# Kernel optimization log

Measured on AMD Instinct MI355X. Metric: run time of the kernel, lower is better.

Reference implementation:

```python
import jax, jax.numpy as jnp
import numpy as np


def kernel_mus(n_kernels):
    l_mu = [1.0]
    if n_kernels == 1:
        return l_mu
    bin_size = 2.0 / (n_kernels - 1)
    l_mu.append(1 - bin_size / 2)
    for i in range(1, n_kernels - 1):
        l_mu.append(l_mu[i] - bin_size)
    return l_mu


def kernel_sigmas(n_kernels):
    bin_size = 2.0 / (n_kernels - 1)
    l_sigma = [0.0001]
    if n_kernels == 1:
        return l_sigma
    l_sigma += [0.5 * bin_size] * (n_kernels - 1)
    return l_sigma


def setup_inputs() -> dict:
    key = jax.random.key(0)
    k0, k1, k2, k3 = jax.random.split(key, 4)
    B, Q, D, E, V, K = 256, 32, 512, 300, 100000, 11
    query_tokens = jax.random.randint(k0, (B, Q), 0, V)
    doc_tokens = jax.random.randint(k1, (B, D), 0, V)
    emb_table = jax.random.normal(k2, (V, E), jnp.float32) * 0.02
    dense_w = jax.random.uniform(k3, (1, K), jnp.float32, -0.014, 0.014)
    dense_b = jnp.zeros((1,), jnp.float32)
    mu = jnp.asarray(kernel_mus(K), jnp.float32)
    sigma = jnp.asarray(kernel_sigmas(K), jnp.float32)
    return {"query_tokens": query_tokens, "doc_tokens": doc_tokens,
            "emb_table": emb_table, "dense_w": dense_w, "dense_b": dense_b,
            "mu": mu, "sigma": sigma}


def reference(query_tokens, doc_tokens, emb_table, dense_w, dense_b, mu, sigma):
    EPS = 1e-13  # CosineMatrixAttention tiny value
    q_mask = (query_tokens > 0).astype(jnp.float32)   # [B,Q]
    d_mask = (doc_tokens > 0).astype(jnp.float32)     # [B,D]
    q_emb = emb_table[query_tokens]                   # [B,Q,E]
    d_emb = emb_table[doc_tokens]                     # [B,D,E]
    q_n = q_emb / (jnp.linalg.norm(q_emb, axis=-1, keepdims=True) + EPS)
    d_n = d_emb / (jnp.linalg.norm(d_emb, axis=-1, keepdims=True) + EPS)
    cosine = jnp.einsum('bqe,bde->bqd', q_n, d_n)     # [B,Q,D]
    pair_mask = q_mask[:, :, None] * d_mask[:, None, :]  # [B,Q,D]
    cosine_masked = cosine * pair_mask
    # gaussian kernels: [B,Q,D,K]
    diff = cosine_masked[..., None] - mu
    kernels = jnp.exp(-(diff * diff) / (2.0 * sigma * sigma)) * pair_mask[..., None]
    per_kernel_query = jnp.sum(kernels, axis=2)       # [B,Q,K]
    log_pkq = jnp.log(jnp.clip(per_kernel_query, 1e-10)) * 0.01
    log_pkq = log_pkq * q_mask[..., None]
    per_kernel = jnp.sum(log_pkq, axis=1)             # [B,K]
    out = per_kernel @ dense_w.T + dense_b            # [B,1]
    return out[:, 0]
```

## Files before the change

kernel.cpp:

```cpp
#include <hip/hip_runtime.h>


#define B      256
#define BQ     32
#define BD     512
#define EDIM   300
#define ROWB   320
#define NK     11
#define QSTR   336

typedef float floatx4 __attribute__((ext_vector_type(4)));

__device__ __forceinline__ float sbc(float x) {
    return __uint_as_float(__builtin_amdgcn_readfirstlane(__float_as_uint(x)));
}

__global__ __launch_bounds__(256)
void knrm_mark(const int* __restrict__ qtok, const int* __restrict__ dtok,
               unsigned char* __restrict__ flags)
{
    int i = blockIdx.x * 256 + threadIdx.x;
    const int NQ = B * BQ;
    const int ND = B * BD;
    if (i < NQ) flags[qtok[i]] = 1;
    else if (i < NQ + ND) flags[dtok[i - NQ]] = 1;
}

__global__ __launch_bounds__(256)
void knrm_norm(const float* __restrict__ emb, const unsigned char* __restrict__ flags,
               unsigned char* __restrict__ ebf, float* __restrict__ rnorm, int V)
{
    int r    = blockIdx.x * 32 + (threadIdx.x >> 3);
    int part = threadIdx.x & 7;
    if (r >= V) return;
    if (!flags[r]) return;
    const float4* src = (const float4*)(emb + (size_t)r * EDIM);
    float v[5][8];
    float mx = 0.f;
    #pragma unroll
    for (int i = 0; i < 5; ++i) {
        int j = part + i * 8;
        #pragma unroll
        for (int t = 0; t < 8; ++t) v[i][t] = 0.f;
        if (j < 37) {
            float4 a = src[2 * j];
            float4 c = src[2 * j + 1];
            v[i][0] = a.x; v[i][1] = a.y; v[i][2] = a.z; v[i][3] = a.w;
            v[i][4] = c.x; v[i][5] = c.y; v[i][6] = c.z; v[i][7] = c.w;
        } else if (j == 37) {
            float4 a = src[74];
            v[i][0] = a.x; v[i][1] = a.y; v[i][2] = a.z; v[i][3] = a.w;
        }
        #pragma unroll
        for (int t = 0; t < 8; ++t) mx = fmaxf(mx, fabsf(v[i][t]));
    }
    mx = fmaxf(mx, __shfl_xor(mx, 1));
    mx = fmaxf(mx, __shfl_xor(mx, 2));
    mx = fmaxf(mx, __shfl_xor(mx, 4));
    float s = (mx > 0.f) ? (64.f / mx) : 0.f;

    float ss = 0.f;
    uint2* dst = (uint2*)(ebf + (size_t)r * ROWB);
    #pragma unroll
    for (int i = 0; i < 5; ++i) {
        int j = part + i * 8;
        unsigned int w0 = 0u, w1 = 0u;
        w0 = __builtin_amdgcn_cvt_pk_fp8_f32(v[i][0] * s, v[i][1] * s, w0, false);
        w0 = __builtin_amdgcn_cvt_pk_fp8_f32(v[i][2] * s, v[i][3] * s, w0, true);
        w1 = __builtin_amdgcn_cvt_pk_fp8_f32(v[i][4] * s, v[i][5] * s, w1, false);
        w1 = __builtin_amdgcn_cvt_pk_fp8_f32(v[i][6] * s, v[i][7] * s, w1, true);
        float g;
        g = __builtin_amdgcn_cvt_f32_fp8(w0, 0); ss += g * g;
        g = __builtin_amdgcn_cvt_f32_fp8(w0, 1); ss += g * g;
        g = __builtin_amdgcn_cvt_f32_fp8(w0, 2); ss += g * g;
        g = __builtin_amdgcn_cvt_f32_fp8(w0, 3); ss += g * g;
        g = __builtin_amdgcn_cvt_f32_fp8(w1, 0); ss += g * g;
        g = __builtin_amdgcn_cvt_f32_fp8(w1, 1); ss += g * g;
        g = __builtin_amdgcn_cvt_f32_fp8(w1, 2); ss += g * g;
        g = __builtin_amdgcn_cvt_f32_fp8(w1, 3); ss += g * g;
        uint2 o; o.x = w0; o.y = w1;
        dst[j] = o;
    }
    ss += __shfl_xor(ss, 1);
    ss += __shfl_xor(ss, 2);
    ss += __shfl_xor(ss, 4);
    if (part == 0) rnorm[r] = 1.f / (sqrtf(ss) + 1e-13f);
}

__device__ __forceinline__ void load_frags(long* bf, const unsigned char* __restrict__ ebf,
                                           int tok, int quad)
{
    const long* src = (const long*)(ebf + (size_t)tok * ROWB);
    #pragma unroll
    for (int ks = 0; ks < 10; ++ks)
        bf[ks] = src[quad + ks * 4];
}

__global__ __launch_bounds__(512, 2)
void knrm_main8(const int* __restrict__ qtok, const int* __restrict__ dtok,
                const unsigned char* __restrict__ ebf, const float* __restrict__ rnorm,
                const float* __restrict__ mu, const float* __restrict__ sigma,
                const float* __restrict__ dw, const float* __restrict__ db,
                float* __restrict__ out)
{
    __shared__ __align__(16) unsigned char q_buf[BQ * QSTR];
    __shared__ float pkq_s[BQ * NK];
    __shared__ float rqs[BQ];
    __shared__ float red[BQ];

    const int tid  = threadIdx.x;
    const int lane = tid & 63;
    const int wv   = tid >> 6;
    const int b    = blockIdx.x;
    const int l16  = lane & 15;
    const int quad = lane >> 4;

    for (int i = tid; i < BQ * NK; i += 512) pkq_s[i] = 0.f;
    if (tid < BQ) rqs[tid] = rnorm[qtok[b * BQ + tid]];

    const int dbase = b * BD + wv * 16 + l16;
    int   td[4];
    float rd[4], dm[4];
    #pragma unroll
    for (int s = 0; s < 4; ++s) {
        td[s] = dtok[dbase + s * 128];
        rd[s] = rnorm[td[s]];
        dm[s] = (td[s] > 0) ? 1.f : 0.f;
    }

    {
        int row = tid >> 4, part = tid & 15;
        int tok = qtok[b * BQ + row];
        const uint4* src  = (const uint4*)(ebf + (size_t)tok * ROWB);
        uint4*       qrow = (uint4*)&q_buf[row * QSTR];
        for (int c = part; c < 20; c += 16) qrow[c] = src[c];
    }

    long bf0[10], bf1[10];
    load_frags(bf0, ebf, td[0], quad);

    __syncthreads();

    float mur[NK], cfr[NK];
    #pragma unroll
    for (int k = 0; k < NK; ++k) {
        float s = sbc(sigma[k]);
        mur[k] = sbc(mu[k]);
        cfr[k] = -0.5f / (s * s);
    }
    float rqv[8];
    #pragma unroll
    for (int slab = 0; slab < 2; ++slab)
        #pragma unroll
        for (int r = 0; r < 4; ++r)
            rqv[slab * 4 + r] = rqs[slab * 16 + quad * 4 + r];

    const unsigned char* a0 = &q_buf[l16 * QSTR + quad * 8];
    const unsigned char* a1 = a0 + 16 * QSTR;

    float pk[2][4][NK];
    #pragma unroll
    for (int slab = 0; slab < 2; ++slab)
        #pragma unroll
        for (int r = 0; r < 4; ++r)
            #pragma unroll
            for (int k = 0; k < NK; ++k) pk[slab][r][k] = 0.f;

    #pragma unroll
    for (int s = 0; s < 4; ++s) {
        const long* bf = (s & 1) ? bf1 : bf0;

        floatx4 acc0 = {0.f, 0.f, 0.f, 0.f};
        floatx4 acc1 = {0.f, 0.f, 0.f, 0.f};
        #pragma unroll
        for (int ks = 0; ks < 10; ++ks) {
            long aA = *(const long*)(a0 + ks * 32);
            long aB = *(const long*)(a1 + ks * 32);
            acc0 = __builtin_amdgcn_mfma_f32_16x16x32_fp8_fp8(aA, bf[ks], acc0, 0, 0, 0);
            acc1 = __builtin_amdgcn_mfma_f32_16x16x32_fp8_fp8(aB, bf[ks], acc1, 0, 0, 0);
        }

        if (s < 3) load_frags((s & 1) ? bf0 : bf1, ebf, td[s + 1], quad);

        #pragma unroll
        for (int slab = 0; slab < 2; ++slab) {
            floatx4 acc = slab ? acc1 : acc0;
            #pragma unroll
            for (int r = 0; r < 4; ++r) {
                float c0 = acc[r] * rqv[slab * 4 + r] * rd[s];
                #pragma unroll
                for (int k = 0; k < NK; ++k) {
                    float d0 = c0 - mur[k];
                    pk[slab][r][k] += dm[s] * __expf(cfr[k] * d0 * d0);
                }
            }
        }
    }

    #pragma unroll
    for (int slab = 0; slab < 2; ++slab)
        #pragma unroll
        for (int r = 0; r < 4; ++r)
            #pragma unroll
            for (int k = 0; k < NK; ++k) {
                float v = pk[slab][r][k];
                v += __shfl_xor(v, 1);
                v += __shfl_xor(v, 2);
                v += __shfl_xor(v, 4);
                v += __shfl_xor(v, 8);
                if (l16 == 0)
                    atomicAdd(&pkq_s[(slab * 16 + quad * 4 + r) * NK + k], v);
            }
    __syncthreads();

    if (tid < BQ) {
        int tok = qtok[b * BQ + tid];
        float sq = 0.f;
        if (tok > 0) {
            #pragma unroll
            for (int k = 0; k < NK; ++k) {
                float s = fmaxf(pkq_s[tid * NK + k], 1e-10f);
                sq += __logf(s) * 0.01f * dw[k];
            }
        }
        red[tid] = sq;
    }
    __syncthreads();
    if (tid == 0) {
        float s = db[0];
        #pragma unroll 8
        for (int i = 0; i < BQ; ++i) s += red[i];
        out[b] = s;
    }
}

extern "C" void kernel_launch(void* const* d_in, const int* in_sizes, int n_in,
                              void* d_out, int out_size, void* d_ws, size_t ws_size,
                              hipStream_t stream)
{
    const int*   qtok  = (const int*)d_in[0];
    const int*   dtok  = (const int*)d_in[1];
    const float* emb   = (const float*)d_in[2];
    const float* dw    = (const float*)d_in[3];
    const float* dbias = (const float*)d_in[4];
    const float* mu    = (const float*)d_in[5];
    const float* sg    = (const float*)d_in[6];
    float* out = (float*)d_out;

    const int V = in_sizes[2] / EDIM;
    const size_t ebf_bytes = (size_t)V * ROWB;
    const size_t rn_bytes  = (size_t)((V * 4 + 255) & ~255);

    unsigned char* ebf   = (unsigned char*)d_ws;
    float*         rnorm = (float*)((char*)d_ws + ebf_bytes);
    unsigned char* flags = (unsigned char*)((char*)d_ws + ebf_bytes + rn_bytes);

    hipMemsetAsync(flags, 0, V, stream);
    const int ntok = B * BQ + B * BD;
    knrm_mark<<<(ntok + 255) / 256, 256, 0, stream>>>(qtok, dtok, flags);
    knrm_norm<<<(V + 31) / 32, 256, 0, stream>>>(emb, flags, ebf, rnorm, V);
    knrm_main8<<<B, 512, 0, stream>>>(qtok, dtok, ebf, rnorm, mu, sg, dw, dbias, out);
}
```

Baseline: 223.5 us.

## Stage doc embeddings through double-buffered LDS with K-permuted row layout

The fp8 row layout written by the norm kernel is permuted so each lane's K-fragments are contiguous. Document rows are now loaded cooperatively with coalesced 16-byte global loads into a double-buffered shared-memory tile, replacing per-lane scattered 8-byte loads straight into registers. MFMA operands are then read as 16-byte LDS vectors. The goal is better global coalescing and latency hiding, at the cost of extra LDS (about 97KB per block, which may limit occupancy to one block per CU) and a barrier per stage.

```diff
diff --git a/kernel.cpp b/kernel.cpp
--- a/kernel.cpp
+++ b/kernel.cpp
@@ -7,9 +7,10 @@
 #define EDIM   300
 #define ROWB   320
 #define NK     11
-#define QSTR   336
+#define DSTR   336
 
 typedef float floatx4 __attribute__((ext_vector_type(4)));
+typedef long  longx2  __attribute__((ext_vector_type(2)));
 
 __device__ __forceinline__ float sbc(float x) {
     return __uint_as_float(__builtin_amdgcn_readfirstlane(__float_as_uint(x)));
@@ -79,7 +80,7 @@
         g = __builtin_amdgcn_cvt_f32_fp8(w1, 2); ss += g * g;
         g = __builtin_amdgcn_cvt_f32_fp8(w1, 3); ss += g * g;
         uint2 o; o.x = w0; o.y = w1;
-        dst[j] = o;
+        dst[(j & 3) * 10 + (j >> 2)] = o;
     }
     ss += __shfl_xor(ss, 1);
     ss += __shfl_xor(ss, 2);
@@ -87,23 +88,42 @@
     if (part == 0) rnorm[r] = 1.f / (sqrtf(ss) + 1e-13f);
 }
 
-__device__ __forceinline__ void load_frags(long* bf, const unsigned char* __restrict__ ebf,
-                                           int tok, int quad)
-{
-    const long* src = (const long*)(ebf + (size_t)tok * ROWB);
-    #pragma unroll
-    for (int ks = 0; ks < 10; ++ks)
-        bf[ks] = src[quad + ks * 4];
+__device__ __forceinline__ void stage_ld(uint4 t0[4], uint4 t1[4],
+        const unsigned char* __restrict__ ebf, const int* __restrict__ dtok_blk,
+        int s, int tid)
+{
+    int part = tid & 15, rr = tid >> 4;
+    #pragma unroll
+    for (int p = 0; p < 4; ++p) {
+        int i = p * 32 + rr;
+        int tok = dtok_blk[s * 128 + i];
+        const uint4* src = (const uint4*)(ebf + (size_t)tok * ROWB);
+        t0[p] = src[part];
+        if (part < 4) t1[p] = src[16 + part];
+    }
+}
+__device__ __forceinline__ void stage_st(const uint4 t0[4], const uint4 t1[4],
+        unsigned char* dst_base, int tid)
+{
+    int part = tid & 15, rr = tid >> 4;
+    #pragma unroll
+    for (int p = 0; p < 4; ++p) {
+        int i = p * 32 + rr;
+        uint4* dst = (uint4*)(dst_base + i * DSTR);
+        dst[part] = t0[p];
+        if (part < 4) dst[16 + part] = t1[p];
+    }
 }
 
 __global__ __launch_bounds__(512, 2)
-void knrm_main8(const int* __restrict__ qtok, const int* __restrict__ dtok,
+void knrm_main9(const int* __restrict__ qtok, const int* __restrict__ dtok,
                 const unsigned char* __restrict__ ebf, const float* __restrict__ rnorm,
                 const float* __restrict__ mu, const float* __restrict__ sigma,
                 const float* __restrict__ dw, const float* __restrict__ db,
                 float* __restrict__ out)
 {
-    __shared__ __align__(16) unsigned char q_buf[BQ * QSTR];
+    __shared__ __align__(16) unsigned char q_buf[BQ * DSTR];
+    __shared__ __align__(16) unsigned char d_buf[2][128 * DSTR];
     __shared__ float pkq_s[BQ * NK];
     __shared__ float rqs[BQ];
     __shared__ float red[BQ];
@@ -114,6 +134,7 @@
     const int b    = blockIdx.x;
     const int l16  = lane & 15;
     const int quad = lane >> 4;
+    const int* dtok_blk = dtok + b * BD;
 
     for (int i = tid; i < BQ * NK; i += 512) pkq_s[i] = 0.f;
     if (tid < BQ) rqs[tid] = rnorm[qtok[b * BQ + tid]];
@@ -128,18 +149,17 @@
         dm[s] = (td[s] > 0) ? 1.f : 0.f;
     }
 
+    uint4 ta[4], tb[4];
+    stage_ld(ta, tb, ebf, dtok_blk, 0, tid);
     {
         int row = tid >> 4, part = tid & 15;
-        int tok = qtok[b * BQ + row];
-        const uint4* src  = (const uint4*)(ebf + (size_t)tok * ROWB);
-        uint4*       qrow = (uint4*)&q_buf[row * QSTR];
-        for (int c = part; c < 20; c += 16) qrow[c] = src[c];
-    }
-
-    long bf0[10], bf1[10];
-    load_frags(bf0, ebf, td[0], quad);
-
-    __syncthreads();
+        int tokq = qtok[b * BQ + row];
+        const uint4* src  = (const uint4*)(ebf + (size_t)tokq * ROWB);
+        uint4*       qrow = (uint4*)&q_buf[row * DSTR];
+        qrow[part] = src[part];
+        if (part < 4) qrow[16 + part] = src[16 + part];
+    }
+    stage_st(ta, tb, d_buf[0], tid);
 
     float mur[NK], cfr[NK];
     #pragma unroll
@@ -148,39 +168,47 @@
         mur[k] = sbc(mu[k]);
         cfr[k] = -0.5f / (s * s);
     }
+
+    float pk[2][4][NK];
+    #pragma unroll
+    for (int slab = 0; slab < 2; ++slab)
+        #pragma unroll
+        for (int r = 0; r < 4; ++r)
+            #pragma unroll
+            for (int k = 0; k < NK; ++k) pk[slab][r][k] = 0.f;
+
+    const unsigned char* a0 = &q_buf[l16 * DSTR + quad * 80];
+    const unsigned char* a1 = a0 + 16 * DSTR;
+
+    int cur = 0;
     float rqv[8];
-    #pragma unroll
-    for (int slab = 0; slab < 2; ++slab)
-        #pragma unroll
-        for (int r = 0; r < 4; ++r)
-            rqv[slab * 4 + r] = rqs[slab * 16 + quad * 4 + r];
-
-    const unsigned char* a0 = &q_buf[l16 * QSTR + quad * 8];
-    const unsigned char* a1 = a0 + 16 * QSTR;
-
-    float pk[2][4][NK];
-    #pragma unroll
-    for (int slab = 0; slab < 2; ++slab)
-        #pragma unroll
-        for (int r = 0; r < 4; ++r)
-            #pragma unroll
-            for (int k = 0; k < NK; ++k) pk[slab][r][k] = 0.f;
 
     #pragma unroll
     for (int s = 0; s < 4; ++s) {
-        const long* bf = (s & 1) ? bf1 : bf0;
-
+        __syncthreads();
+
+        if (s < 3) stage_ld(ta, tb, ebf, dtok_blk, s + 1, tid);
+        if (s == 0) {
+            #pragma unroll
+            for (int slab = 0; slab < 2; ++slab)
+                #pragma unroll
+                for (int r = 0; r < 4; ++r)
+                    rqv[slab * 4 + r] = rqs[slab * 16 + quad * 4 + r];
+        }
+
+        const unsigned char* bp = d_buf[cur] + (wv * 16 + l16) * DSTR + quad * 80;
         floatx4 acc0 = {0.f, 0.f, 0.f, 0.f};
         floatx4 acc1 = {0.f, 0.f, 0.f, 0.f};
         #pragma unroll
-        for (int ks = 0; ks < 10; ++ks) {
-            long aA = *(const long*)(a0 + ks * 32);
-            long aB = *(const long*)(a1 + ks * 32);
-            acc0 = __builtin_amdgcn_mfma_f32_16x16x32_fp8_fp8(aA, bf[ks], acc0, 0, 0, 0);
-            acc1 = __builtin_amdgcn_mfma_f32_16x16x32_fp8_fp8(aB, bf[ks], acc1, 0, 0, 0);
-        }
-
-        if (s < 3) load_frags((s & 1) ? bf0 : bf1, ebf, td[s + 1], quad);
+        for (int k2 = 0; k2 < 5; ++k2) {
+            longx2 vA0 = *(const longx2*)(a0 + k2 * 16);
+            longx2 vA1 = *(const longx2*)(a1 + k2 * 16);
+            longx2 vB  = *(const longx2*)(bp + k2 * 16);
+            acc0 = __builtin_amdgcn_mfma_f32_16x16x32_fp8_fp8(vA0.x, vB.x, acc0, 0, 0, 0);
+            acc0 = __builtin_amdgcn_mfma_f32_16x16x32_fp8_fp8(vA0.y, vB.y, acc0, 0, 0, 0);
+            acc1 = __builtin_amdgcn_mfma_f32_16x16x32_fp8_fp8(vA1.x, vB.x, acc1, 0, 0, 0);
+            acc1 = __builtin_amdgcn_mfma_f32_16x16x32_fp8_fp8(vA1.y, vB.y, acc1, 0, 0, 0);
+        }
 
         #pragma unroll
         for (int slab = 0; slab < 2; ++slab) {
@@ -195,6 +223,9 @@
                 }
             }
         }
+
+        if (s < 3) stage_st(ta, tb, d_buf[cur ^ 1], tid);
+        cur ^= 1;
     }
 
     #pragma unroll
@@ -259,5 +290,5 @@
     const int ntok = B * BQ + B * BD;
     knrm_mark<<<(ntok + 255) / 256, 256, 0, stream>>>(qtok, dtok, flags);
     knrm_norm<<<(V + 31) / 32, 256, 0, stream>>>(emb, flags, ebf, rnorm, V);
-    knrm_main8<<<B, 512, 0, stream>>>(qtok, dtok, ebf, rnorm, mu, sg, dw, dbias, out);
-}
+    knrm_main9<<<B, 512, 0, stream>>>(qtok, dtok, ebf, rnorm, mu, sg, dw, dbias, out);
+}
```

Measured after the change: 246.4 us. 1.1x slower.
